# Optimization experiments

Hardware: AMD Instinct MI355X
Metric: run time of the kernel (lower is better)

## Reference

```python
import jax, jax.numpy as jnp
import numpy as np

EPS = 1e-5


def setup_inputs() -> dict:
    key = jax.random.key(0)
    k1, k2, k3, k4 = jax.random.split(key, 4)
    B, C, H, W = 32, 256, 64, 64
    x_real = jax.random.normal(k1, (B, C, H, W), dtype=jnp.float32)
    x_imag = jax.random.normal(k2, (B, C, H, W), dtype=jnp.float32)
    # per-channel 2x2 affine weight and 2-vector bias (module init is
    # 0.7071*I and zeros; we perturb so gradients are non-trivial)
    weight = (0.70710678 * jnp.eye(2, dtype=jnp.float32)[:, :, None]
              + 0.05 * jax.random.normal(k3, (2, 2, C), dtype=jnp.float32))
    bias = 0.05 * jax.random.normal(k4, (2, C), dtype=jnp.float32)
    return {"x_real": x_real, "x_imag": x_imag, "weight": weight, "bias": bias}


def reference(x_real, x_imag, weight, bias):
    # Complex BatchNorm (training-mode batch statistics).
    # x_*: [B, C, H, W]; stats reduced over (B, H, W) per channel C.
    axes = (0, 2, 3)
    mu_r = jnp.mean(x_real, axes)  # [C]
    mu_i = jnp.mean(x_imag, axes)  # [C]
    xr = x_real - mu_r[None, :, None, None]
    xi = x_imag - mu_i[None, :, None, None]

    # 2x2 covariance per channel, eps on the diagonal
    Vrr = jnp.mean(xr * xr, axes) + EPS  # [C]
    Vii = jnp.mean(xi * xi, axes) + EPS  # [C]
    Vri = jnp.mean(xr * xi, axes)        # [C]

    # Analytic inverse square root of the 2x2 SPD matrix [[Vrr,Vri],[Vri,Vii]]
    s = jnp.sqrt(Vrr * Vii - Vri * Vri)       # sqrt(det)
    t = jnp.sqrt(Vrr + Vii + 2.0 * s)         # sqrt(trace + 2 sqrt(det))
    inv_st = 1.0 / (s * t)
    Rrr = (Vii + s) * inv_st
    Rii = (Vrr + s) * inv_st
    Rri = -Vri * inv_st

    # Whitening (per-channel 2x2 matmul on (real, imag))
    cb = lambda v: v[None, :, None, None]
    xhat_r = cb(Rrr) * xr + cb(Rri) * xi
    xhat_i = cb(Rri) * xr + cb(Rii) * xi

    # Affine: out = W @ xhat + b, W: [2,2,C], b: [2,C]
    out_r = cb(weight[0, 0]) * xhat_r + cb(weight[0, 1]) * xhat_i + cb(bias[0])
    out_i = cb(weight[1, 0]) * xhat_r + cb(weight[1, 1]) * xhat_i + cb(bias[1])
    return jnp.stack([out_r, out_i], axis=0)  # [2, B, C, H, W]
```

## Files before the change

### kernel.cpp

```cpp
#include <hip/hip_runtime.h>
#include <math.h>

#define C_CH   256
#define HW     4096
#define B_N    32
#define BC     (B_N * C_CH)
#define N_PER_CH (B_N * HW)
#define N_TOT  ((size_t)BC * HW)
#define EPS_BN 1e-5f

typedef float f32x4 __attribute__((ext_vector_type(4)));

__global__ __launch_bounds__(256) void cbn_partials(
    const float* __restrict__ xr, const float* __restrict__ xi,
    float* __restrict__ part)
{
    const int bc = blockIdx.x;
    const int t  = threadIdx.x;
    const f32x4* r4 = reinterpret_cast<const f32x4*>(xr + (size_t)bc * HW);
    const f32x4* i4 = reinterpret_cast<const f32x4*>(xi + (size_t)bc * HW);

    float sr = 0.f, si = 0.f, srr = 0.f, sii = 0.f, sri = 0.f;
#pragma unroll
    for (int k = 0; k < (HW / 4) / 256; ++k) {
        f32x4 a = r4[t + k * 256];
        f32x4 b = i4[t + k * 256];
        sr  += a.x + a.y + a.z + a.w;
        si  += b.x + b.y + b.z + b.w;
        srr += a.x * a.x + a.y * a.y + a.z * a.z + a.w * a.w;
        sii += b.x * b.x + b.y * b.y + b.z * b.z + b.w * b.w;
        sri += a.x * b.x + a.y * b.y + a.z * b.z + a.w * b.w;
    }

#pragma unroll
    for (int off = 32; off > 0; off >>= 1) {
        sr  += __shfl_down(sr,  off);
        si  += __shfl_down(si,  off);
        srr += __shfl_down(srr, off);
        sii += __shfl_down(sii, off);
        sri += __shfl_down(sri, off);
    }

    __shared__ float red[5][4];
    const int wave = t >> 6;
    if ((t & 63) == 0) {
        red[0][wave] = sr;  red[1][wave] = si;
        red[2][wave] = srr; red[3][wave] = sii; red[4][wave] = sri;
    }
    __syncthreads();
    if (t == 0) {
        part[0 * BC + bc] = red[0][0] + red[0][1] + red[0][2] + red[0][3];
        part[1 * BC + bc] = red[1][0] + red[1][1] + red[1][2] + red[1][3];
        part[2 * BC + bc] = red[2][0] + red[2][1] + red[2][2] + red[2][3];
        part[3 * BC + bc] = red[3][0] + red[3][1] + red[3][2] + red[3][3];
        part[4 * BC + bc] = red[4][0] + red[4][1] + red[4][2] + red[4][3];
    }
}

__global__ __launch_bounds__(256) void cbn_apply(
    const float* __restrict__ xr, const float* __restrict__ xi,
    const float* __restrict__ part,
    const float* __restrict__ weight,
    const float* __restrict__ bias,
    float* __restrict__ out)
{
    const int bc = (BC - 1) - blockIdx.x;
    const int c  = bc & (C_CH - 1);
    const int t  = threadIdx.x;

    __shared__ float scoef[6];

    if (t < 64) {
        float sr = 0.f, si = 0.f, srr = 0.f, sii = 0.f, sri = 0.f;
        if (t < 32) {
            const int idx = t * C_CH + c;
            sr  = part[0 * BC + idx];
            si  = part[1 * BC + idx];
            srr = part[2 * BC + idx];
            sii = part[3 * BC + idx];
            sri = part[4 * BC + idx];
        }
#pragma unroll
        for (int off = 16; off > 0; off >>= 1) {
            sr  += __shfl_down(sr,  off);
            si  += __shfl_down(si,  off);
            srr += __shfl_down(srr, off);
            sii += __shfl_down(sii, off);
            sri += __shfl_down(sri, off);
        }
        if (t == 0) {
            const float invN = 1.0f / (float)N_PER_CH;
            const float mur = sr * invN;
            const float mui = si * invN;
            const float Vrr = srr * invN - mur * mur + EPS_BN;
            const float Vii = sii * invN - mui * mui + EPS_BN;
            const float Vri = sri * invN - mur * mui;

            const float s      = sqrtf(Vrr * Vii - Vri * Vri);
            const float tt     = sqrtf(Vrr + Vii + 2.0f * s);
            const float inv_st = 1.0f / (s * tt);
            const float Rrr = (Vii + s) * inv_st;
            const float Rii = (Vrr + s) * inv_st;
            const float Rri = -Vri * inv_st;

            const float w00 = weight[0 * C_CH + c];
            const float w01 = weight[1 * C_CH + c];
            const float w10 = weight[2 * C_CH + c];
            const float w11 = weight[3 * C_CH + c];
            const float b0  = bias[c];
            const float b1  = bias[C_CH + c];

            const float Ar = w00 * Rrr + w01 * Rri;
            const float Br = w00 * Rri + w01 * Rii;
            const float Ai = w10 * Rrr + w11 * Rri;
            const float Bi = w10 * Rri + w11 * Rii;

            scoef[0] = Ar;
            scoef[1] = Br;
            scoef[2] = b0 - Ar * mur - Br * mui;
            scoef[3] = Ai;
            scoef[4] = Bi;
            scoef[5] = b1 - Ai * mur - Bi * mui;
        }
    }
    __syncthreads();

    const float Ar = scoef[0], Br = scoef[1], Cr = scoef[2];
    const float Ai = scoef[3], Bi = scoef[4], Ci = scoef[5];

    const size_t base = (size_t)bc * HW;
    const f32x4* r4 = reinterpret_cast<const f32x4*>(xr + base);
    const f32x4* i4 = reinterpret_cast<const f32x4*>(xi + base);
    f32x4* o4r = reinterpret_cast<f32x4*>(out + base);
    f32x4* o4i = reinterpret_cast<f32x4*>(out + N_TOT + base);

#pragma unroll
    for (int k = 0; k < (HW / 4) / 256; ++k) {
        const int j = t + k * 256;
        const f32x4 a = r4[j];
        const f32x4 b = i4[j];
        f32x4 u, v;
        u.x = Ar * a.x + Br * b.x + Cr;
        u.y = Ar * a.y + Br * b.y + Cr;
        u.z = Ar * a.z + Br * b.z + Cr;
        u.w = Ar * a.w + Br * b.w + Cr;
        v.x = Ai * a.x + Bi * b.x + Ci;
        v.y = Ai * a.y + Bi * b.y + Ci;
        v.z = Ai * a.z + Bi * b.z + Ci;
        v.w = Ai * a.w + Bi * b.w + Ci;
        __builtin_nontemporal_store(u, &o4r[j]);
        __builtin_nontemporal_store(v, &o4i[j]);
    }
}

extern "C" void kernel_launch(void* const* d_in, const int* in_sizes, int n_in,
                              void* d_out, int out_size, void* d_ws, size_t ws_size,
                              hipStream_t stream) {
    const float* xr     = (const float*)d_in[0];
    const float* xi     = (const float*)d_in[1];
    const float* weight = (const float*)d_in[2];
    const float* bias   = (const float*)d_in[3];
    float* out = (float*)d_out;

    float* part = (float*)d_ws;

    cbn_partials<<<BC, 256, 0, stream>>>(xr, xi, part);
    cbn_apply<<<BC, 256, 0, stream>>>(xr, xi, part, weight, bias, out);
}
```

Before: 121.6 us.

## Fuse stats and apply into one per-channel kernel with 1024-thread blocks

After: 121.1 us. No clear change (-0.4%).

```diff
diff --git a/kernel.cpp b/kernel.cpp
--- a/kernel.cpp
+++ b/kernel.cpp
@@ -4,27 +4,29 @@
 #define C_CH   256
 #define HW     4096
 #define B_N    32
-#define BC     (B_N * C_CH)
 #define N_PER_CH (B_N * HW)
-#define N_TOT  ((size_t)BC * HW)
+#define N_TOT  ((size_t)B_N * C_CH * HW)
 #define EPS_BN 1e-5f
 
 typedef float f32x4 __attribute__((ext_vector_type(4)));
 
-__global__ __launch_bounds__(256) void cbn_partials(
+__global__ __launch_bounds__(1024) void cbn_fused(
     const float* __restrict__ xr, const float* __restrict__ xi,
-    float* __restrict__ part)
+    const float* __restrict__ weight,
+    const float* __restrict__ bias,
+    float* __restrict__ out)
 {
-    const int bc = blockIdx.x;
-    const int t  = threadIdx.x;
-    const f32x4* r4 = reinterpret_cast<const f32x4*>(xr + (size_t)bc * HW);
-    const f32x4* i4 = reinterpret_cast<const f32x4*>(xi + (size_t)bc * HW);
+    const int c = blockIdx.x;
+    const int t = threadIdx.x;
+    const f32x4* r4 = reinterpret_cast<const f32x4*>(xr);
+    const f32x4* i4 = reinterpret_cast<const f32x4*>(xi);
 
     float sr = 0.f, si = 0.f, srr = 0.f, sii = 0.f, sri = 0.f;
-#pragma unroll
-    for (int k = 0; k < (HW / 4) / 256; ++k) {
-        f32x4 a = r4[t + k * 256];
-        f32x4 b = i4[t + k * 256];
+#pragma unroll 4
+    for (int j = 0; j < B_N; ++j) {
+        const size_t idx = ((size_t)(j * C_CH + c) << 10) + t;
+        const f32x4 a = r4[idx];
+        const f32x4 b = i4[idx];
         sr  += a.x + a.y + a.z + a.w;
         si  += b.x + b.y + b.z + b.w;
         srr += a.x * a.x + a.y * a.y + a.z * a.z + a.w * a.w;
@@ -41,60 +43,36 @@
         sri += __shfl_down(sri, off);
     }
 
-    __shared__ float red[5][4];
+    __shared__ float red[5][16];
+    __shared__ float scoef[6];
     const int wave = t >> 6;
     if ((t & 63) == 0) {
         red[0][wave] = sr;  red[1][wave] = si;
         red[2][wave] = srr; red[3][wave] = sii; red[4][wave] = sri;
     }
     __syncthreads();
-    if (t == 0) {
-        part[0 * BC + bc] = red[0][0] + red[0][1] + red[0][2] + red[0][3];
-        part[1 * BC + bc] = red[1][0] + red[1][1] + red[1][2] + red[1][3];
-        part[2 * BC + bc] = red[2][0] + red[2][1] + red[2][2] + red[2][3];
-        part[3 * BC + bc] = red[3][0] + red[3][1] + red[3][2] + red[3][3];
-        part[4 * BC + bc] = red[4][0] + red[4][1] + red[4][2] + red[4][3];
-    }
-}
-
-__global__ __launch_bounds__(256) void cbn_apply(
-    const float* __restrict__ xr, const float* __restrict__ xi,
-    const float* __restrict__ part,
-    const float* __restrict__ weight,
-    const float* __restrict__ bias,
-    float* __restrict__ out)
-{
-    const int bc = (BC - 1) - blockIdx.x;
-    const int c  = bc & (C_CH - 1);
-    const int t  = threadIdx.x;
-
-    __shared__ float scoef[6];
 
     if (t < 64) {
-        float sr = 0.f, si = 0.f, srr = 0.f, sii = 0.f, sri = 0.f;
-        if (t < 32) {
-            const int idx = t * C_CH + c;
-            sr  = part[0 * BC + idx];
-            si  = part[1 * BC + idx];
-            srr = part[2 * BC + idx];
-            sii = part[3 * BC + idx];
-            sri = part[4 * BC + idx];
+        float v0 = 0.f, v1 = 0.f, v2 = 0.f, v3 = 0.f, v4 = 0.f;
+        if (t < 16) {
+            v0 = red[0][t]; v1 = red[1][t]; v2 = red[2][t];
+            v3 = red[3][t]; v4 = red[4][t];
         }
 #pragma unroll
-        for (int off = 16; off > 0; off >>= 1) {
-            sr  += __shfl_down(sr,  off);
-            si  += __shfl_down(si,  off);
-            srr += __shfl_down(srr, off);
-            sii += __shfl_down(sii, off);
-            sri += __shfl_down(sri, off);
+        for (int off = 8; off > 0; off >>= 1) {
+            v0 += __shfl_down(v0, off);
+            v1 += __shfl_down(v1, off);
+            v2 += __shfl_down(v2, off);
+            v3 += __shfl_down(v3, off);
+            v4 += __shfl_down(v4, off);
         }
         if (t == 0) {
             const float invN = 1.0f / (float)N_PER_CH;
-            const float mur = sr * invN;
-            const float mui = si * invN;
-            const float Vrr = srr * invN - mur * mur + EPS_BN;
-            const float Vii = sii * invN - mui * mui + EPS_BN;
-            const float Vri = sri * invN - mur * mui;
+            const float mur = v0 * invN;
+            const float mui = v1 * invN;
+            const float Vrr = v2 * invN - mur * mur + EPS_BN;
+            const float Vii = v3 * invN - mui * mui + EPS_BN;
+            const float Vri = v4 * invN - mur * mui;
 
             const float s      = sqrtf(Vrr * Vii - Vri * Vri);
             const float tt     = sqrtf(Vrr + Vii + 2.0f * s);
@@ -128,17 +106,14 @@
     const float Ar = scoef[0], Br = scoef[1], Cr = scoef[2];
     const float Ai = scoef[3], Bi = scoef[4], Ci = scoef[5];
 
-    const size_t base = (size_t)bc * HW;
-    const f32x4* r4 = reinterpret_cast<const f32x4*>(xr + base);
-    const f32x4* i4 = reinterpret_cast<const f32x4*>(xi + base);
-    f32x4* o4r = reinterpret_cast<f32x4*>(out + base);
-    f32x4* o4i = reinterpret_cast<f32x4*>(out + N_TOT + base);
+    f32x4* o4 = reinterpret_cast<f32x4*>(out);
+    const size_t n4 = N_TOT / 4;
 
-#pragma unroll
-    for (int k = 0; k < (HW / 4) / 256; ++k) {
-        const int j = t + k * 256;
-        const f32x4 a = r4[j];
-        const f32x4 b = i4[j];
+#pragma unroll 4
+    for (int j = 0; j < B_N; ++j) {
+        const size_t idx = ((size_t)(j * C_CH + c) << 10) + t;
+        const f32x4 a = __builtin_nontemporal_load(&r4[idx]);
+        const f32x4 b = __builtin_nontemporal_load(&i4[idx]);
         f32x4 u, v;
         u.x = Ar * a.x + Br * b.x + Cr;
         u.y = Ar * a.y + Br * b.y + Cr;
@@ -148,8 +123,8 @@
         v.y = Ai * a.y + Bi * b.y + Ci;
         v.z = Ai * a.z + Bi * b.z + Ci;
         v.w = Ai * a.w + Bi * b.w + Ci;
-        __builtin_nontemporal_store(u, &o4r[j]);
-        __builtin_nontemporal_store(v, &o4i[j]);
+        __builtin_nontemporal_store(u, &o4[idx]);
+        __builtin_nontemporal_store(v, &o4[n4 + idx]);
     }
 }
 
@@ -162,8 +137,5 @@
     const float* bias   = (const float*)d_in[3];
     float* out = (float*)d_out;
 
-    float* part = (float*)d_ws;
-
-    cbn_partials<<<BC, 256, 0, stream>>>(xr, xi, part);
-    cbn_apply<<<BC, 256, 0, stream>>>(xr, xi, part, weight, bias, out);
+    cbn_fused<<<C_CH, 1024, 0, stream>>>(xr, xi, weight, bias, out);
 }
```
